# Kernel tuning notes

Hardware: AMD Instinct MI355X
Metric: run time of the kernel (lower is better)

The kernel has to match this reference:

```python
import jax, jax.numpy as jnp
import numpy as np

N_ATOMS = 50000
N_EDGES = 1_600_000
N_MOL = 500
HIDDEN = 128
FILTERS = 128
GAUSS = 50
LAYERS = 3
CUTOFF = 10.0
LOG2 = 0.6931471805599453


def ssp(x):
    # ShiftedSoftplus: softplus(x) - log(2)
    return jax.nn.softplus(x) - LOG2


def setup_inputs() -> dict:
    key = jax.random.key(0)
    ks = jax.random.split(key, 24)
    z = jax.random.randint(ks[0], (N_ATOMS,), 0, 100)
    pos = jax.random.uniform(ks[1], (N_ATOMS, 3), jnp.float32) * 5.0  # box keeps d < cutoff
    batch = jnp.sort(jax.random.randint(ks[2], (N_ATOMS,), 0, N_MOL))
    row = jax.random.randint(ks[3], (N_EDGES,), 0, N_ATOMS)
    off = jax.random.randint(ks[4], (N_EDGES,), 1, N_ATOMS)
    col = (row + off) % N_ATOMS  # guarantees row != col (no zero distances)
    edge_index = jnp.stack([row, col])
    def lin(k, fi, fo):
        return jax.random.normal(k, (fi, fo), jnp.float32) * (1.0 / np.sqrt(fi))
    emb = jax.random.normal(ks[5], (100, HIDDEN), jnp.float32)
    mlp1_w = jnp.stack([lin(jax.random.fold_in(ks[6], i), GAUSS, FILTERS) for i in range(LAYERS)])
    mlp1_b = jnp.zeros((LAYERS, FILTERS), jnp.float32)
    mlp2_w = jnp.stack([lin(jax.random.fold_in(ks[7], i), FILTERS, FILTERS) for i in range(LAYERS)])
    mlp2_b = jnp.zeros((LAYERS, FILTERS), jnp.float32)
    lin1_w = jnp.stack([lin(jax.random.fold_in(ks[8], i), HIDDEN, FILTERS) for i in range(LAYERS)])
    lin2_w = jnp.stack([lin(jax.random.fold_in(ks[9], i), FILTERS, HIDDEN) for i in range(LAYERS)])
    lin2_b = jnp.zeros((LAYERS, HIDDEN), jnp.float32)
    int_w = jnp.stack([lin(jax.random.fold_in(ks[10], i), HIDDEN, HIDDEN) for i in range(LAYERS)])
    int_b = jnp.zeros((LAYERS, HIDDEN), jnp.float32)
    out1_w = lin(ks[11], HIDDEN, HIDDEN // 2)
    out1_b = jnp.zeros((HIDDEN // 2,), jnp.float32)
    out2_w = lin(ks[12], HIDDEN // 2, 1)
    out2_b = jnp.zeros((1,), jnp.float32)
    return {"z": z, "pos": pos, "batch": batch, "edge_index": edge_index,
            "emb": emb, "mlp1_w": mlp1_w, "mlp1_b": mlp1_b, "mlp2_w": mlp2_w, "mlp2_b": mlp2_b,
            "lin1_w": lin1_w, "lin2_w": lin2_w, "lin2_b": lin2_b, "int_w": int_w, "int_b": int_b,
            "out1_w": out1_w, "out1_b": out1_b, "out2_w": out2_w, "out2_b": out2_b}


def reference(z, pos, batch, edge_index, emb, mlp1_w, mlp1_b, mlp2_w, mlp2_b,
              lin1_w, lin2_w, lin2_b, int_w, int_b, out1_w, out1_b, out2_w, out2_b):
    row, col = edge_index[0], edge_index[1]  # source j, target i
    d = jnp.linalg.norm(pos[row] - pos[col], axis=-1)  # [E]
    # GaussianSmearing
    offset = jnp.linspace(0.0, CUTOFF, GAUSS)
    coeff = -0.5 / (offset[1] - offset[0]) ** 2
    rbf = jnp.exp(coeff * (d[:, None] - offset[None, :]) ** 2)  # [E, GAUSS]
    # cosine cutoff
    C = 0.5 * (jnp.cos(d * jnp.pi / CUTOFF) + 1.0)  # [E]
    h = emb[z]  # [N, H]
    for l in range(LAYERS):
        W = ssp(rbf @ mlp1_w[l] + mlp1_b[l]) @ mlp2_w[l] + mlp2_b[l]  # [E, F]
        W = W * C[:, None]
        x = h @ lin1_w[l]                 # [N, F]
        msg = x[row] * W                  # gather from source, per-edge filter
        agg = jax.ops.segment_sum(msg, col, num_segments=N_ATOMS)  # scatter-add to targets
        x = agg @ lin2_w[l] + lin2_b[l]
        x = ssp(x)
        x = x @ int_w[l] + int_b[l]
        h = h + x                         # residual
    h = ssp(h @ out1_w + out1_b)
    h = h @ out2_w + out2_b               # [N, 1] per-atom energy
    out = jax.ops.segment_sum(h[:, 0], batch, num_segments=N_MOL)  # 'add' readout
    return out.reshape(-1)
```

## Files before the change

kernel.cpp:

```cpp
#include <hip/hip_runtime.h>
#include <math.h>

#define HID 128
#define NGAUSS 50
#define TBL 2048
#define TBL2 8192
#define DMAX 8.6605f
#define LDX 136

typedef _Float16 h4 __attribute__((ext_vector_type(4)));
typedef _Float16 f16x8 __attribute__((ext_vector_type(8)));
typedef float f32x4 __attribute__((ext_vector_type(4)));

__device__ __forceinline__ float sspf(float x) {
  float ax = fabsf(x);
  return fmaxf(x, 0.0f) + log1pf(expf(-ax)) - 0.69314718055994530942f;
}

__global__ __launch_bounds__(128) void build_table_k(
    const float* __restrict__ w1, const float* __restrict__ b1,
    const float* __restrict__ w2, const float* __restrict__ b2,
    float* __restrict__ tab) {
  int l = blockIdx.x >> 11;
  int ti = blockIdx.x & (TBL - 1);
  int j = threadIdx.x;
  __shared__ float rbf[NGAUSS];
  __shared__ float v1[HID];
  const float step = DMAX / (float)(TBL - 1);
  float d = ti * step;
  if (j < NGAUSS) {
    const float gstep = 10.0f / 49.0f;
    const float gcoeff = -12.005f;
    float diff = d - j * gstep;
    rbf[j] = expf(gcoeff * diff * diff);
  }
  __syncthreads();
  float s = b1[l * HID + j];
  const float* w1p = w1 + l * NGAUSS * HID + j;
  for (int g = 0; g < NGAUSS; g++) s = fmaf(rbf[g], w1p[g * HID], s);
  v1[j] = sspf(s);
  __syncthreads();
  float s2 = b2[l * HID + j];
  const float* w2p = w2 + l * HID * HID + j;
  for (int k = 0; k < HID; k++) s2 = fmaf(v1[k], w2p[k * HID], s2);
  float C = 0.5f * (cosf(d * 0.3141592653589793f) + 1.0f);
  tab[((size_t)l * TBL + ti) * HID + j] = s2 * C;
}

__global__ __launch_bounds__(256) void upsample_k(
    const float* __restrict__ tab, _Float16* __restrict__ tabh) {
  int idx = blockIdx.x * 256 + threadIdx.x;
  if (idx >= 3 * TBL2 * HID) return;
  int ch = idx & 127;
  int i = (idx >> 7) & (TBL2 - 1);
  int l = idx >> 20;
  float t = (float)i * ((float)(TBL - 1) / (float)(TBL2 - 1));
  int i0 = min((int)t, TBL - 2);
  float f = t - (float)i0;
  const float* base = tab + ((size_t)l * TBL + i0) * HID + ch;
  tabh[idx] = (_Float16)fmaf(f, base[HID] - base[0], base[0]);
}

__global__ __launch_bounds__(256) void wtrans10_k(
    const float* __restrict__ lin1, const float* __restrict__ lin2,
    const float* __restrict__ intw, const float* __restrict__ out1w,
    _Float16* __restrict__ out) {
  int b = blockIdx.x;
  __shared__ _Float16 tile[128 * 130];
  int t = threadIdx.x;
  if (b < 9) {
    const float* src = (b < 3 ? lin1 : (b < 6 ? lin2 : intw)) + (size_t)(b % 3) * HID * HID;
    _Float16* dst = out + (size_t)b * HID * HID;
    for (int i = t; i < HID * HID; i += 256) tile[(i >> 7) * 130 + (i & 127)] = (_Float16)src[i];
    __syncthreads();
    for (int i = t; i < HID * HID; i += 256) dst[i] = tile[(i & 127) * 130 + (i >> 7)];
  } else {
    _Float16* dst = out + (size_t)9 * HID * HID;
    for (int i = t; i < 128 * 64; i += 256) tile[(i >> 6) * 66 + (i & 63)] = (_Float16)out1w[i];
    __syncthreads();
    for (int i = t; i < 64 * 128; i += 256) dst[i] = tile[(i & 127) * 66 + (i >> 7)];
  }
}

__global__ __launch_bounds__(256) void bcount_k(
    const int* __restrict__ col, int* __restrict__ bcount, int E, int nbuck) {
  __shared__ int hist[1024];
  int t = threadIdx.x;
  int e0 = blockIdx.x * 2048;
  for (int j = t; j < nbuck; j += 256) hist[j] = 0;
  __syncthreads();
#pragma unroll
  for (int u = 0; u < 8; u++) {
    int e = e0 + u * 256 + t;
    if (e < E) atomicAdd(&hist[col[e] >> 6], 1);
  }
  __syncthreads();
  for (int j = t; j < nbuck; j += 256)
    if (hist[j]) atomicAdd(&bcount[j], hist[j]);
}

__global__ __launch_bounds__(256) void bucket_scan_k(
    const int* __restrict__ bcount, int* __restrict__ bstart,
    int* __restrict__ bcur, int nbuck, int* __restrict__ starts, int N) {
  __shared__ int sh[256];
  int t = threadIdx.x;
  int chunk = (nbuck + 255) / 256;
  int b0 = t * chunk;
  int c[8];
  int s = 0;
  for (int j = 0; j < chunk; j++) {
    int idx = b0 + j;
    int v = (idx < nbuck) ? bcount[idx] : 0;
    c[j] = v;
    s += v;
  }
  sh[t] = s;
  __syncthreads();
  for (int o = 1; o < 256; o <<= 1) {
    int v = (t >= o) ? sh[t - o] : 0;
    __syncthreads();
    sh[t] += v;
    __syncthreads();
  }
  int p = (t == 0) ? 0 : sh[t - 1];
  for (int j = 0; j < chunk; j++) {
    int idx = b0 + j;
    if (idx < nbuck) {
      bstart[idx] = p;
      bcur[idx] = p;
      p += c[j];
    }
  }
  if (t == 255) {
    bstart[nbuck] = p;
    starts[N] = p;
  }
}

__global__ __launch_bounds__(256) void scatterA_k(
    const int* __restrict__ row, const int* __restrict__ col,
    const float* __restrict__ pos, int* __restrict__ bcur,
    unsigned long long* __restrict__ tmp, int E, int nbuck) {
  __shared__ int hist[1024];
  __shared__ int base[1024];
  int t = threadIdx.x;
  int e0 = blockIdx.x * 2048;
  for (int j = t; j < nbuck; j += 256) hist[j] = 0;
  __syncthreads();
  int bkt[8];
  int rnk[8];
  unsigned long long key[8];
#pragma unroll
  for (int u = 0; u < 8; u++) {
    int e = e0 + u * 256 + t;
    bkt[u] = -1;
    if (e < E) {
      int r = row[e], c = col[e];
      float dx = pos[r * 3 + 0] - pos[c * 3 + 0];
      float dy = pos[r * 3 + 1] - pos[c * 3 + 1];
      float dz = pos[r * 3 + 2] - pos[c * 3 + 2];
      float d = sqrtf(dx * dx + dy * dy + dz * dz);
      const float inv2 = (float)(TBL2 - 1) / DMAX;
      int q = min((int)(d * inv2 + 0.5f), TBL2 - 1);
      unsigned int pay = ((unsigned int)r << 13) | (unsigned int)q;
      key[u] = ((unsigned long long)pay << 6) | (unsigned long long)(c & 63);
      bkt[u] = c >> 6;
      rnk[u] = atomicAdd(&hist[bkt[u]], 1);
    }
  }
  __syncthreads();
  for (int j = t; j < nbuck; j += 256)
    base[j] = hist[j] ? atomicAdd(&bcur[j], hist[j]) : 0;
  __syncthreads();
#pragma unroll
  for (int u = 0; u < 8; u++)
    if (bkt[u] >= 0) tmp[(size_t)base[bkt[u]] + rnk[u]] = key[u];
}

__global__ __launch_bounds__(256) void scatterB_k(
    const unsigned long long* __restrict__ tmp, const int* __restrict__ bstart,
    int* __restrict__ starts, unsigned int* __restrict__ payload, int N) {
  int j = blockIdx.x;
  int t = threadIdx.x;
  __shared__ int cnt[64];
  __shared__ int cur[64];
  int rs = bstart[j], re = bstart[j + 1];
  if (t < 64) cnt[t] = 0;
  __syncthreads();
  for (int e = rs + t; e < re; e += 256)
    atomicAdd(&cnt[(int)(tmp[e] & 63)], 1);
  __syncthreads();
  if (t < 64) {
    int mine = cnt[t];
    int v = mine;
    for (int o = 1; o < 64; o <<= 1) {
      int u = __shfl_up(v, o, 64);
      if (t >= o) v += u;
    }
    int excl = v - mine;
    int c = j * 64 + t;
    if (c < N) starts[c] = rs + excl;
    cur[t] = rs + excl;
  }
  __syncthreads();
  for (int e = rs + t; e < re; e += 256) {
    unsigned long long k = tmp[e];
    int p = atomicAdd(&cur[(int)(k & 63)], 1);
    payload[p] = (unsigned int)(k >> 6);
  }
}


__global__ __launch_bounds__(256) void lin1_emb_k(
    const int* __restrict__ z, const float* __restrict__ emb,
    const _Float16* __restrict__ W1t, float* __restrict__ h,
    _Float16* __restrict__ x16, int N) {
  __shared__ __align__(16) _Float16 Xs[32 * LDX];
  __shared__ __align__(16) _Float16 Ys[32 * LDX];
  __shared__ int zi[32];
  int t = threadIdx.x;
  int lane = t & 63, w = t >> 6;
  int g = w & 1, c = w >> 1;
  int mrow = lane & 15, quad = lane >> 4;
  int a0 = blockIdx.x * 32;
  if (t < 32) zi[t] = (a0 + t < N) ? z[a0 + t] : 0;
  __syncthreads();
#pragma unroll
  for (int p = 0; p < 4; p++) {
    int id = t + p * 256;
    int a = id >> 5, kg = id & 31;
    float4 v = ((const float4*)emb)[(size_t)zi[a] * 32 + kg];
    if (a0 + a < N) ((float4*)h)[(size_t)(a0 + a) * 32 + kg] = v;
    h4 o;
    o.x = (_Float16)v.x; o.y = (_Float16)v.y;
    o.z = (_Float16)v.z; o.w = (_Float16)v.w;
    *(h4*)&Xs[a * LDX + kg * 4] = o;
  }
  __syncthreads();
  f16x8 af[4];
#pragma unroll
  for (int kk = 0; kk < 4; kk++)
    af[kk] = *(const f16x8*)&Xs[(g * 16 + mrow) * LDX + kk * 32 + quad * 8];
  f32x4 zero = {0.f, 0.f, 0.f, 0.f};
  f32x4 acc[4];
#pragma unroll
  for (int i = 0; i < 4; i++) acc[i] = zero;
#pragma unroll
  for (int kk = 0; kk < 4; kk++) {
    f16x8 bf[4];
#pragma unroll
    for (int nt = 0; nt < 4; nt++)
      bf[nt] = *(const f16x8*)(W1t + (size_t)(c * 64 + nt * 16 + mrow) * HID + kk * 32 + quad * 8);
#pragma unroll
    for (int nt = 0; nt < 4; nt++)
      acc[nt] = __builtin_amdgcn_mfma_f32_16x16x32_f16(af[kk], bf[nt], acc[nt], 0, 0, 0);
  }
#pragma unroll
  for (int nt = 0; nt < 4; nt++) {
    int colv = c * 64 + nt * 16 + mrow;
#pragma unroll
    for (int r = 0; r < 4; r++)
      Ys[(g * 16 + quad * 4 + r) * LDX + colv] = (_Float16)acc[nt][r];
  }
  __syncthreads();
#pragma unroll
  for (int p = 0; p < 2; p++) {
    int id = t + p * 256;
    int a = id >> 4, kg = id & 15;
    if (a0 + a < N)
      ((uint4*)x16)[(size_t)(a0 + a) * 16 + kg] = *(uint4*)&Ys[a * LDX + kg * 8];
  }
}

__global__ __launch_bounds__(256) void fused_mid_k(
    const _Float16* __restrict__ agg16, const _Float16* __restrict__ W2t,
    const float* __restrict__ b2, const _Float16* __restrict__ W3t,
    const float* __restrict__ b3, float* __restrict__ h,
    const _Float16* __restrict__ W1nt, _Float16* __restrict__ x16, int N) {
  __shared__ __align__(16) _Float16 Xs[32 * LDX];
  __shared__ __align__(16) _Float16 Ys[32 * LDX];
  int t = threadIdx.x;
  int lane = t & 63, w = t >> 6;
  int g = w & 1, c = w >> 1;
  int mrow = lane & 15, quad = lane >> 4;
  int a0 = blockIdx.x * 32;
#pragma unroll
  for (int p = 0; p < 2; p++) {
    int id = t + p * 256;
    int a = id >> 4, kg = id & 15;
    uint4 v = make_uint4(0, 0, 0, 0);
    if (a0 + a < N) v = ((const uint4*)agg16)[(size_t)(a0 + a) * 16 + kg];
    *(uint4*)&Xs[a * LDX + kg * 8] = v;
  }
  __syncthreads();
  f32x4 zero = {0.f, 0.f, 0.f, 0.f};
  f16x8 af[4];
  f32x4 acc[4];
#pragma unroll
  for (int kk = 0; kk < 4; kk++)
    af[kk] = *(const f16x8*)&Xs[(g * 16 + mrow) * LDX + kk * 32 + quad * 8];
#pragma unroll
  for (int i = 0; i < 4; i++) acc[i] = zero;
#pragma unroll
  for (int kk = 0; kk < 4; kk++) {
    f16x8 bf[4];
#pragma unroll
    for (int nt = 0; nt < 4; nt++)
      bf[nt] = *(const f16x8*)(W2t + (size_t)(c * 64 + nt * 16 + mrow) * HID + kk * 32 + quad * 8);
#pragma unroll
    for (int nt = 0; nt < 4; nt++)
      acc[nt] = __builtin_amdgcn_mfma_f32_16x16x32_f16(af[kk], bf[nt], acc[nt], 0, 0, 0);
  }
#pragma unroll
  for (int nt = 0; nt < 4; nt++) {
    int colv = c * 64 + nt * 16 + mrow;
    float bb = b2[colv];
#pragma unroll
    for (int r = 0; r < 4; r++)
      Ys[(g * 16 + quad * 4 + r) * LDX + colv] = (_Float16)sspf(acc[nt][r] + bb);
  }
  __syncthreads();
#pragma unroll
  for (int kk = 0; kk < 4; kk++)
    af[kk] = *(const f16x8*)&Ys[(g * 16 + mrow) * LDX + kk * 32 + quad * 8];
#pragma unroll
  for (int i = 0; i < 4; i++) acc[i] = zero;
#pragma unroll
  for (int kk = 0; kk < 4; kk++) {
    f16x8 bf[4];
#pragma unroll
    for (int nt = 0; nt < 4; nt++)
      bf[nt] = *(const f16x8*)(W3t + (size_t)(c * 64 + nt * 16 + mrow) * HID + kk * 32 + quad * 8);
#pragma unroll
    for (int nt = 0; nt < 4; nt++)
      acc[nt] = __builtin_amdgcn_mfma_f32_16x16x32_f16(af[kk], bf[nt], acc[nt], 0, 0, 0);
  }
#pragma unroll
  for (int nt = 0; nt < 4; nt++) {
    int colv = c * 64 + nt * 16 + mrow;
    float bb = b3[colv];
#pragma unroll
    for (int r = 0; r < 4; r++)
      Xs[(g * 16 + quad * 4 + r) * LDX + colv] = (_Float16)(acc[nt][r] + bb);
  }
  __syncthreads();
#pragma unroll
  for (int p = 0; p < 4; p++) {
    int id = t + p * 256;
    int a = id >> 5, kg = id & 31;
    h4 xv = *(h4*)&Xs[a * LDX + kg * 4];
    float4 v = make_float4((float)xv.x, (float)xv.y, (float)xv.z, (float)xv.w);
    if (a0 + a < N) {
      float4 ho = ((const float4*)h)[(size_t)(a0 + a) * 32 + kg];
      v.x += ho.x; v.y += ho.y; v.z += ho.z; v.w += ho.w;
      ((float4*)h)[(size_t)(a0 + a) * 32 + kg] = v;
    }
    h4 o;
    o.x = (_Float16)v.x; o.y = (_Float16)v.y;
    o.z = (_Float16)v.z; o.w = (_Float16)v.w;
    *(h4*)&Xs[a * LDX + kg * 4] = o;
  }
  __syncthreads();
#pragma unroll
  for (int kk = 0; kk < 4; kk++)
    af[kk] = *(const f16x8*)&Xs[(g * 16 + mrow) * LDX + kk * 32 + quad * 8];
#pragma unroll
  for (int i = 0; i < 4; i++) acc[i] = zero;
#pragma unroll
  for (int kk = 0; kk < 4; kk++) {
    f16x8 bf[4];
#pragma unroll
    for (int nt = 0; nt < 4; nt++)
      bf[nt] = *(const f16x8*)(W1nt + (size_t)(c * 64 + nt * 16 + mrow) * HID + kk * 32 + quad * 8);
#pragma unroll
    for (int nt = 0; nt < 4; nt++)
      acc[nt] = __builtin_amdgcn_mfma_f32_16x16x32_f16(af[kk], bf[nt], acc[nt], 0, 0, 0);
  }
#pragma unroll
  for (int nt = 0; nt < 4; nt++) {
    int colv = c * 64 + nt * 16 + mrow;
#pragma unroll
    for (int r = 0; r < 4; r++)
      Ys[(g * 16 + quad * 4 + r) * LDX + colv] = (_Float16)acc[nt][r];
  }
  __syncthreads();
#pragma unroll
  for (int p = 0; p < 2; p++) {
    int id = t + p * 256;
    int a = id >> 4, kg = id & 15;
    if (a0 + a < N)
      ((uint4*)x16)[(size_t)(a0 + a) * 16 + kg] = *(uint4*)&Ys[a * LDX + kg * 8];
  }
}

__global__ __launch_bounds__(256) void fused_last_k(
    const _Float16* __restrict__ agg16, const _Float16* __restrict__ W2t,
    const float* __restrict__ b2, const _Float16* __restrict__ W3t,
    const float* __restrict__ b3, const float* __restrict__ h,
    const _Float16* __restrict__ Wo1t, const float* __restrict__ o1b,
    const float* __restrict__ o2w, const float* __restrict__ o2b,
    const int* __restrict__ batch, float* __restrict__ out, int N) {
  __shared__ __align__(16) _Float16 Xs[32 * LDX];
  __shared__ __align__(16) _Float16 Ys[32 * LDX];
  __shared__ float ebuf[32];
  int t = threadIdx.x;
  int lane = t & 63, w = t >> 6;
  int g = w & 1, c = w >> 1;
  int mrow = lane & 15, quad = lane >> 4;
  int a0 = blockIdx.x * 32;
  if (t < 32) ebuf[t] = 0.f;
#pragma unroll
  for (int p = 0; p < 2; p++) {
    int id = t + p * 256;
    int a = id >> 4, kg = id & 15;
    uint4 v = make_uint4(0, 0, 0, 0);
    if (a0 + a < N) v = ((const uint4*)agg16)[(size_t)(a0 + a) * 16 + kg];
    *(uint4*)&Xs[a * LDX + kg * 8] = v;
  }
  __syncthreads();
  f32x4 zero = {0.f, 0.f, 0.f, 0.f};
  f16x8 af[4];
  f32x4 acc[4];
#pragma unroll
  for (int kk = 0; kk < 4; kk++)
    af[kk] = *(const f16x8*)&Xs[(g * 16 + mrow) * LDX + kk * 32 + quad * 8];
#pragma unroll
  for (int i = 0; i < 4; i++) acc[i] = zero;
#pragma unroll
  for (int kk = 0; kk < 4; kk++) {
    f16x8 bf[4];
#pragma unroll
    for (int nt = 0; nt < 4; nt++)
      bf[nt] = *(const f16x8*)(W2t + (size_t)(c * 64 + nt * 16 + mrow) * HID + kk * 32 + quad * 8);
#pragma unroll
    for (int nt = 0; nt < 4; nt++)
      acc[nt] = __builtin_amdgcn_mfma_f32_16x16x32_f16(af[kk], bf[nt], acc[nt], 0, 0, 0);
  }
#pragma unroll
  for (int nt = 0; nt < 4; nt++) {
    int colv = c * 64 + nt * 16 + mrow;
    float bb = b2[colv];
#pragma unroll
    for (int r = 0; r < 4; r++)
      Ys[(g * 16 + quad * 4 + r) * LDX + colv] = (_Float16)sspf(acc[nt][r] + bb);
  }
  __syncthreads();
#pragma unroll
  for (int kk = 0; kk < 4; kk++)
    af[kk] = *(const f16x8*)&Ys[(g * 16 + mrow) * LDX + kk * 32 + quad * 8];
#pragma unroll
  for (int i = 0; i < 4; i++) acc[i] = zero;
#pragma unroll
  for (int kk = 0; kk < 4; kk++) {
    f16x8 bf[4];
#pragma unroll
    for (int nt = 0; nt < 4; nt++)
      bf[nt] = *(const f16x8*)(W3t + (size_t)(c * 64 + nt * 16 + mrow) * HID + kk * 32 + quad * 8);
#pragma unroll
    for (int nt = 0; nt < 4; nt++)
      acc[nt] = __builtin_amdgcn_mfma_f32_16x16x32_f16(af[kk], bf[nt], acc[nt], 0, 0, 0);
  }
#pragma unroll
  for (int nt = 0; nt < 4; nt++) {
    int colv = c * 64 + nt * 16 + mrow;
    float bb = b3[colv];
#pragma unroll
    for (int r = 0; r < 4; r++)
      Xs[(g * 16 + quad * 4 + r) * LDX + colv] = (_Float16)(acc[nt][r] + bb);
  }
  __syncthreads();
#pragma unroll
  for (int p = 0; p < 4; p++) {
    int id = t + p * 256;
    int a = id >> 5, kg = id & 31;
    h4 xv = *(h4*)&Xs[a * LDX + kg * 4];
    float4 v = make_float4((float)xv.x, (float)xv.y, (float)xv.z, (float)xv.w);
    if (a0 + a < N) {
      float4 ho = ((const float4*)h)[(size_t)(a0 + a) * 32 + kg];
      v.x += ho.x; v.y += ho.y; v.z += ho.z; v.w += ho.w;
    }
    h4 o;
    o.x = (_Float16)v.x; o.y = (_Float16)v.y;
    o.z = (_Float16)v.z; o.w = (_Float16)v.w;
    *(h4*)&Xs[a * LDX + kg * 4] = o;
  }
  __syncthreads();
#pragma unroll
  for (int kk = 0; kk < 4; kk++)
    af[kk] = *(const f16x8*)&Xs[(g * 16 + mrow) * LDX + kk * 32 + quad * 8];
#pragma unroll
  for (int i = 0; i < 2; i++) acc[i] = zero;
#pragma unroll
  for (int kk = 0; kk < 4; kk++) {
    f16x8 bf[2];
#pragma unroll
    for (int nt = 0; nt < 2; nt++)
      bf[nt] = *(const f16x8*)(Wo1t + (size_t)(c * 32 + nt * 16 + mrow) * HID + kk * 32 + quad * 8);
#pragma unroll
    for (int nt = 0; nt < 2; nt++)
      acc[nt] = __builtin_amdgcn_mfma_f32_16x16x32_f16(af[kk], bf[nt], acc[nt], 0, 0, 0);
  }
  float ss[4] = {0.f, 0.f, 0.f, 0.f};
#pragma unroll
  for (int nt = 0; nt < 2; nt++) {
    int colv = c * 32 + nt * 16 + mrow;
    float bb = o1b[colv];
    float ww = o2w[colv];
#pragma unroll
    for (int r = 0; r < 4; r++) ss[r] += sspf(acc[nt][r] + bb) * ww;
  }
#pragma unroll
  for (int r = 0; r < 4; r++) {
    ss[r] += __shfl_xor(ss[r], 1);
    ss[r] += __shfl_xor(ss[r], 2);
    ss[r] += __shfl_xor(ss[r], 4);
    ss[r] += __shfl_xor(ss[r], 8);
    if (mrow == 0) atomicAdd(&ebuf[g * 16 + quad * 4 + r], ss[r]);
  }
  __syncthreads();
  if (t < 32) {
    int a = a0 + t;
    if (a < N) atomicAdd(&out[batch[a]], ebuf[t] + o2b[0]);
  }
}

__global__ __launch_bounds__(256) void aggregate_k(
    const int* __restrict__ starts, const unsigned int* __restrict__ payload,
    const _Float16* __restrict__ x16, const _Float16* __restrict__ tabh,
    _Float16* __restrict__ agg16, int N) {
  int a = blockIdx.x * 4 + (threadIdx.x >> 6);
  if (a >= N) return;
  int lane = threadIdx.x & 63;
  int half = lane >> 5;
  int sl = lane & 31;
  int s = starts[a], e_end = starts[a + 1];
  float4 acc0 = make_float4(0.f, 0.f, 0.f, 0.f);
  float4 acc1 = make_float4(0.f, 0.f, 0.f, 0.f);
  auto do_edge = [&](unsigned int p, float4& acc) {
    int tq = (int)(p & 8191u);
    int r = (int)(p >> 13);
    h4 tw = *(const h4*)&tabh[(size_t)tq * HID + sl * 4];
    h4 xr = *(const h4*)&x16[(size_t)r * HID + sl * 4];
    acc.x = fmaf((float)xr.x, (float)tw.x, acc.x);
    acc.y = fmaf((float)xr.y, (float)tw.y, acc.y);
    acc.z = fmaf((float)xr.z, (float)tw.z, acc.z);
    acc.w = fmaf((float)xr.w, (float)tw.w, acc.w);
  };
  int i = s;
  for (; i + 8 <= e_end; i += 8) {
    unsigned int p0 = payload[i + half];
    unsigned int p1 = payload[i + 2 + half];
    unsigned int p2 = payload[i + 4 + half];
    unsigned int p3 = payload[i + 6 + half];
    do_edge(p0, acc0);
    do_edge(p1, acc1);
    do_edge(p2, acc0);
    do_edge(p3, acc1);
  }
  for (; i < e_end; i += 2) {
    int e = i + half;
    if (e < e_end) do_edge(payload[e], acc0);
  }
  acc0.x += acc1.x; acc0.y += acc1.y; acc0.z += acc1.z; acc0.w += acc1.w;
  acc0.x += __shfl_xor(acc0.x, 32);
  acc0.y += __shfl_xor(acc0.y, 32);
  acc0.z += __shfl_xor(acc0.z, 32);
  acc0.w += __shfl_xor(acc0.w, 32);
  if (half == 0) {
    h4 o;
    o.x = (_Float16)acc0.x; o.y = (_Float16)acc0.y;
    o.z = (_Float16)acc0.z; o.w = (_Float16)acc0.w;
    *(h4*)&agg16[(size_t)a * HID + sl * 4] = o;
  }
}

extern "C" void kernel_launch(void* const* d_in, const int* in_sizes, int n_in,
                              void* d_out, int out_size, void* d_ws, size_t ws_size,
                              hipStream_t stream) {
  const int* z = (const int*)d_in[0];
  const float* pos = (const float*)d_in[1];
  const int* batch = (const int*)d_in[2];
  const int* eidx = (const int*)d_in[3];
  const float* emb = (const float*)d_in[4];
  const float* mlp1_w = (const float*)d_in[5];
  const float* mlp1_b = (const float*)d_in[6];
  const float* mlp2_w = (const float*)d_in[7];
  const float* mlp2_b = (const float*)d_in[8];
  const float* lin1_w = (const float*)d_in[9];
  const float* lin2_w = (const float*)d_in[10];
  const float* lin2_b = (const float*)d_in[11];
  const float* int_w = (const float*)d_in[12];
  const float* int_b = (const float*)d_in[13];
  const float* out1_w = (const float*)d_in[14];
  const float* out1_b = (const float*)d_in[15];
  const float* out2_w = (const float*)d_in[16];
  const float* out2_b = (const float*)d_in[17];
  float* out = (float*)d_out;

  const int N = in_sizes[0];
  const int E = in_sizes[3] / 2;
  const int* row = eidx;
  const int* col = eidx + E;
  const int nbuck = (N + 63) / 64;

  char* ws = (char*)d_ws;
  size_t off = 0;
  auto alloc = [&](size_t bytes) -> void* {
    void* p = ws + off;
    off = (off + bytes + 255) & ~(size_t)255;
    return p;
  };
  float* h = (float*)alloc((size_t)N * HID * 4);
  _Float16* x16 = (_Float16*)alloc((size_t)N * HID * 2);
  size_t agg_bytes = (size_t)N * HID * 2;
  size_t tmp_bytes = (size_t)E * 8 + 16;
  void* agg_union = alloc(agg_bytes > tmp_bytes ? agg_bytes : tmp_bytes);
  _Float16* agg16 = (_Float16*)agg_union;
  unsigned long long* tmp = (unsigned long long*)agg_union;
  unsigned int* payload = (unsigned int*)alloc((size_t)E * 4 + 16);
  int* starts = (int*)alloc((size_t)(N + 1) * 4);
  int* bcount = (int*)alloc((size_t)nbuck * 4);
  int* bstart = (int*)alloc((size_t)(nbuck + 1) * 4);
  int* bcur = (int*)alloc((size_t)nbuck * 4);
  float* tab = (float*)alloc((size_t)3 * TBL * HID * 4);
  _Float16* tabh = (_Float16*)alloc((size_t)3 * TBL2 * HID * 2);
  _Float16* Wt10 = (_Float16*)alloc((size_t)10 * HID * HID * 2);
  (void)ws_size;

  hipMemsetAsync(bcount, 0, (size_t)nbuck * 4, stream);
  hipMemsetAsync(out, 0, (size_t)out_size * 4, stream);

  build_table_k<<<3 * TBL, 128, 0, stream>>>(mlp1_w, mlp1_b, mlp2_w, mlp2_b, tab);
  upsample_k<<<(3 * TBL2 * HID + 255) / 256, 256, 0, stream>>>(tab, tabh);
  wtrans10_k<<<10, 256, 0, stream>>>(lin1_w, lin2_w, int_w, out1_w, Wt10);
  bcount_k<<<(E + 2047) / 2048, 256, 0, stream>>>(col, bcount, E, nbuck);
  bucket_scan_k<<<1, 256, 0, stream>>>(bcount, bstart, bcur, nbuck, starts, N);
  scatterA_k<<<(E + 2047) / 2048, 256, 0, stream>>>(row, col, pos, bcur, tmp, E, nbuck);
  scatterB_k<<<nbuck, 256, 0, stream>>>(tmp, bstart, starts, payload, N);

  int g32 = (N + 31) / 32;
  lin1_emb_k<<<g32, 256, 0, stream>>>(z, emb, Wt10, h, x16, N);
  for (int l = 0; l < 2; l++) {
    aggregate_k<<<(N + 3) / 4, 256, 0, stream>>>(starts, payload, x16,
                                                 tabh + (size_t)l * TBL2 * HID, agg16, N);
    fused_mid_k<<<g32, 256, 0, stream>>>(
        agg16, Wt10 + (size_t)(3 + l) * HID * HID, lin2_b + (size_t)l * HID,
        Wt10 + (size_t)(6 + l) * HID * HID, int_b + (size_t)l * HID, h,
        Wt10 + (size_t)(l + 1) * HID * HID, x16, N);
  }
  aggregate_k<<<(N + 3) / 4, 256, 0, stream>>>(starts, payload, x16,
                                               tabh + (size_t)2 * TBL2 * HID, agg16, N);
  fused_last_k<<<g32, 256, 0, stream>>>(
      agg16, Wt10 + (size_t)5 * HID * HID, lin2_b + (size_t)2 * HID,
      Wt10 + (size_t)8 * HID * HID, int_b + (size_t)2 * HID, h,
      Wt10 + (size_t)9 * HID * HID, out1_b, out2_w, out2_b, batch, out, N);
}
```

Measured before the change: 617.5 us.

## Split fused node GEMMs into persistent kernels with LDS-resident swizzled weights

Weights are pre-swizzled into per-lane MFMA fragment order so each persistent block can load a whole 128x128 fp16 matrix into LDS once and reuse it across many 32-atom tiles. This replaces reading B fragments from global memory for every tile. The previously fused mid/last kernels are split into separate lin1, ssp, residual and energy kernels, and the embedding gather becomes its own kernel. The split adds launches and extra HBM round trips of intermediates (x16, h read/written more often) in exchange for weight reuse and fewer blocks.

```diff
diff --git a/kernel.cpp b/kernel.cpp
--- a/kernel.cpp
+++ b/kernel.cpp
@@ -7,6 +7,7 @@
 #define TBL2 8192
 #define DMAX 8.6605f
 #define LDX 136
+#define PGRID 768
 
 typedef _Float16 h4 __attribute__((ext_vector_type(4)));
 typedef _Float16 f16x8 __attribute__((ext_vector_type(8)));
@@ -61,25 +62,45 @@
   tabh[idx] = (_Float16)fmaf(f, base[HID] - base[0], base[0]);
 }
 
-__global__ __launch_bounds__(256) void wtrans10_k(
+__global__ __launch_bounds__(256) void wswz10_k(
     const float* __restrict__ lin1, const float* __restrict__ lin2,
     const float* __restrict__ intw, const float* __restrict__ out1w,
     _Float16* __restrict__ out) {
   int b = blockIdx.x;
-  __shared__ _Float16 tile[128 * 130];
   int t = threadIdx.x;
   if (b < 9) {
     const float* src = (b < 3 ? lin1 : (b < 6 ? lin2 : intw)) + (size_t)(b % 3) * HID * HID;
-    _Float16* dst = out + (size_t)b * HID * HID;
-    for (int i = t; i < HID * HID; i += 256) tile[(i >> 7) * 130 + (i & 127)] = (_Float16)src[i];
-    __syncthreads();
-    for (int i = t; i < HID * HID; i += 256) dst[i] = tile[(i & 127) * 130 + (i >> 7)];
+    _Float16* dst = out + (size_t)b * 16384;
+    for (int i = t; i < 16384; i += 256) {
+      int j = i & 7;
+      int lane = (i >> 3) & 63;
+      int kk = (i >> 9) & 3;
+      int ntc = i >> 11;
+      int n = ntc * 16 + (lane & 15);
+      int k = kk * 32 + (lane >> 4) * 8 + j;
+      dst[i] = (_Float16)src[k * HID + n];
+    }
   } else {
-    _Float16* dst = out + (size_t)9 * HID * HID;
-    for (int i = t; i < 128 * 64; i += 256) tile[(i >> 6) * 66 + (i & 63)] = (_Float16)out1w[i];
-    __syncthreads();
-    for (int i = t; i < 64 * 128; i += 256) dst[i] = tile[(i & 127) * 66 + (i >> 7)];
-  }
+    _Float16* dst = out + (size_t)9 * 16384;
+    for (int i = t; i < 8192; i += 256) {
+      int j = i & 7;
+      int lane = (i >> 3) & 63;
+      int kk = (i >> 9) & 3;
+      int ntc = i >> 11;
+      int n = ntc * 16 + (lane & 15);
+      int k = kk * 32 + (lane >> 4) * 8 + j;
+      dst[i] = (_Float16)out1w[k * 64 + n];
+    }
+  }
+}
+
+__global__ __launch_bounds__(256) void emb_gather_k(
+    const int* __restrict__ z, const float* __restrict__ emb,
+    float* __restrict__ h, int N) {
+  int i4 = blockIdx.x * 256 + threadIdx.x;
+  if (i4 >= N * 32) return;
+  int a = i4 >> 5;
+  ((float4*)h)[i4] = ((const float4*)emb)[z[a] * 32 + (i4 & 31)];
 }
 
 __global__ __launch_bounds__(256) void bcount_k(
@@ -211,316 +232,270 @@
 }
 
 
-__global__ __launch_bounds__(256) void lin1_emb_k(
-    const int* __restrict__ z, const float* __restrict__ emb,
-    const _Float16* __restrict__ W1t, float* __restrict__ h,
-    _Float16* __restrict__ x16, int N) {
+__global__ __launch_bounds__(256) void lin1_p_k(
+    const float* __restrict__ h, const _Float16* __restrict__ Wsw,
+    _Float16* __restrict__ x16, int N, int ntiles) {
+  __shared__ __align__(16) _Float16 Ws[16384];
   __shared__ __align__(16) _Float16 Xs[32 * LDX];
   __shared__ __align__(16) _Float16 Ys[32 * LDX];
-  __shared__ int zi[32];
   int t = threadIdx.x;
   int lane = t & 63, w = t >> 6;
   int g = w & 1, c = w >> 1;
   int mrow = lane & 15, quad = lane >> 4;
-  int a0 = blockIdx.x * 32;
-  if (t < 32) zi[t] = (a0 + t < N) ? z[a0 + t] : 0;
-  __syncthreads();
-#pragma unroll
-  for (int p = 0; p < 4; p++) {
-    int id = t + p * 256;
-    int a = id >> 5, kg = id & 31;
-    float4 v = ((const float4*)emb)[(size_t)zi[a] * 32 + kg];
-    if (a0 + a < N) ((float4*)h)[(size_t)(a0 + a) * 32 + kg] = v;
-    h4 o;
-    o.x = (_Float16)v.x; o.y = (_Float16)v.y;
-    o.z = (_Float16)v.z; o.w = (_Float16)v.w;
-    *(h4*)&Xs[a * LDX + kg * 4] = o;
-  }
-  __syncthreads();
-  f16x8 af[4];
-#pragma unroll
-  for (int kk = 0; kk < 4; kk++)
-    af[kk] = *(const f16x8*)&Xs[(g * 16 + mrow) * LDX + kk * 32 + quad * 8];
+#pragma unroll
+  for (int p = 0; p < 8; p++)
+    ((uint4*)Ws)[t + p * 256] = ((const uint4*)Wsw)[t + p * 256];
+  __syncthreads();
   f32x4 zero = {0.f, 0.f, 0.f, 0.f};
-  f32x4 acc[4];
-#pragma unroll
-  for (int i = 0; i < 4; i++) acc[i] = zero;
-#pragma unroll
-  for (int kk = 0; kk < 4; kk++) {
-    f16x8 bf[4];
-#pragma unroll
-    for (int nt = 0; nt < 4; nt++)
-      bf[nt] = *(const f16x8*)(W1t + (size_t)(c * 64 + nt * 16 + mrow) * HID + kk * 32 + quad * 8);
-#pragma unroll
-    for (int nt = 0; nt < 4; nt++)
-      acc[nt] = __builtin_amdgcn_mfma_f32_16x16x32_f16(af[kk], bf[nt], acc[nt], 0, 0, 0);
-  }
-#pragma unroll
-  for (int nt = 0; nt < 4; nt++) {
-    int colv = c * 64 + nt * 16 + mrow;
-#pragma unroll
-    for (int r = 0; r < 4; r++)
-      Ys[(g * 16 + quad * 4 + r) * LDX + colv] = (_Float16)acc[nt][r];
-  }
-  __syncthreads();
-#pragma unroll
-  for (int p = 0; p < 2; p++) {
-    int id = t + p * 256;
-    int a = id >> 4, kg = id & 15;
-    if (a0 + a < N)
-      ((uint4*)x16)[(size_t)(a0 + a) * 16 + kg] = *(uint4*)&Ys[a * LDX + kg * 8];
-  }
-}
-
-__global__ __launch_bounds__(256) void fused_mid_k(
-    const _Float16* __restrict__ agg16, const _Float16* __restrict__ W2t,
-    const float* __restrict__ b2, const _Float16* __restrict__ W3t,
-    const float* __restrict__ b3, float* __restrict__ h,
-    const _Float16* __restrict__ W1nt, _Float16* __restrict__ x16, int N) {
+  for (int tile = blockIdx.x; tile < ntiles; tile += gridDim.x) {
+    int a0 = tile * 32;
+#pragma unroll
+    for (int p = 0; p < 4; p++) {
+      int id = t + p * 256;
+      int a = id >> 5, kg = id & 31;
+      float4 v = make_float4(0.f, 0.f, 0.f, 0.f);
+      if (a0 + a < N) v = ((const float4*)h)[(size_t)(a0 + a) * 32 + kg];
+      h4 o;
+      o.x = (_Float16)v.x; o.y = (_Float16)v.y;
+      o.z = (_Float16)v.z; o.w = (_Float16)v.w;
+      *(h4*)&Xs[a * LDX + kg * 4] = o;
+    }
+    __syncthreads();
+    f16x8 af[4];
+#pragma unroll
+    for (int kk = 0; kk < 4; kk++)
+      af[kk] = *(const f16x8*)&Xs[(g * 16 + mrow) * LDX + kk * 32 + quad * 8];
+    f32x4 acc[4];
+#pragma unroll
+    for (int i = 0; i < 4; i++) acc[i] = zero;
+#pragma unroll
+    for (int kk = 0; kk < 4; kk++) {
+#pragma unroll
+      for (int nt = 0; nt < 4; nt++) {
+        f16x8 bf = *(const f16x8*)&Ws[(((c * 4 + nt) * 4 + kk) << 9) + lane * 8];
+        acc[nt] = __builtin_amdgcn_mfma_f32_16x16x32_f16(af[kk], bf, acc[nt], 0, 0, 0);
+      }
+    }
+#pragma unroll
+    for (int nt = 0; nt < 4; nt++) {
+      int colv = c * 64 + nt * 16 + mrow;
+#pragma unroll
+      for (int r = 0; r < 4; r++)
+        Ys[(g * 16 + quad * 4 + r) * LDX + colv] = (_Float16)acc[nt][r];
+    }
+    __syncthreads();
+#pragma unroll
+    for (int p = 0; p < 2; p++) {
+      int id = t + p * 256;
+      int a = id >> 4, kg = id & 15;
+      if (a0 + a < N)
+        ((uint4*)x16)[(size_t)(a0 + a) * 16 + kg] = *(uint4*)&Ys[a * LDX + kg * 8];
+    }
+  }
+}
+
+__global__ __launch_bounds__(256) void ssp_p_k(
+    const _Float16* __restrict__ agg16, const _Float16* __restrict__ Wsw,
+    const float* __restrict__ bias, _Float16* __restrict__ y16, int N, int ntiles) {
+  __shared__ __align__(16) _Float16 Ws[16384];
   __shared__ __align__(16) _Float16 Xs[32 * LDX];
   __shared__ __align__(16) _Float16 Ys[32 * LDX];
   int t = threadIdx.x;
   int lane = t & 63, w = t >> 6;
   int g = w & 1, c = w >> 1;
   int mrow = lane & 15, quad = lane >> 4;
-  int a0 = blockIdx.x * 32;
-#pragma unroll
-  for (int p = 0; p < 2; p++) {
-    int id = t + p * 256;
-    int a = id >> 4, kg = id & 15;
-    uint4 v = make_uint4(0, 0, 0, 0);
-    if (a0 + a < N) v = ((const uint4*)agg16)[(size_t)(a0 + a) * 16 + kg];
-    *(uint4*)&Xs[a * LDX + kg * 8] = v;
-  }
+#pragma unroll
+  for (int p = 0; p < 8; p++)
+    ((uint4*)Ws)[t + p * 256] = ((const uint4*)Wsw)[t + p * 256];
+  float br[4];
+#pragma unroll
+  for (int nt = 0; nt < 4; nt++) br[nt] = bias[c * 64 + nt * 16 + mrow];
   __syncthreads();
   f32x4 zero = {0.f, 0.f, 0.f, 0.f};
-  f16x8 af[4];
-  f32x4 acc[4];
-#pragma unroll
-  for (int kk = 0; kk < 4; kk++)
-    af[kk] = *(const f16x8*)&Xs[(g * 16 + mrow) * LDX + kk * 32 + quad * 8];
-#pragma unroll
-  for (int i = 0; i < 4; i++) acc[i] = zero;
-#pragma unroll
-  for (int kk = 0; kk < 4; kk++) {
-    f16x8 bf[4];
-#pragma unroll
-    for (int nt = 0; nt < 4; nt++)
-      bf[nt] = *(const f16x8*)(W2t + (size_t)(c * 64 + nt * 16 + mrow) * HID + kk * 32 + quad * 8);
-#pragma unroll
-    for (int nt = 0; nt < 4; nt++)
-      acc[nt] = __builtin_amdgcn_mfma_f32_16x16x32_f16(af[kk], bf[nt], acc[nt], 0, 0, 0);
-  }
-#pragma unroll
-  for (int nt = 0; nt < 4; nt++) {
-    int colv = c * 64 + nt * 16 + mrow;
-    float bb = b2[colv];
-#pragma unroll
-    for (int r = 0; r < 4; r++)
-      Ys[(g * 16 + quad * 4 + r) * LDX + colv] = (_Float16)sspf(acc[nt][r] + bb);
-  }
-  __syncthreads();
-#pragma unroll
-  for (int kk = 0; kk < 4; kk++)
-    af[kk] = *(const f16x8*)&Ys[(g * 16 + mrow) * LDX + kk * 32 + quad * 8];
-#pragma unroll
-  for (int i = 0; i < 4; i++) acc[i] = zero;
-#pragma unroll
-  for (int kk = 0; kk < 4; kk++) {
-    f16x8 bf[4];
-#pragma unroll
-    for (int nt = 0; nt < 4; nt++)
-      bf[nt] = *(const f16x8*)(W3t + (size_t)(c * 64 + nt * 16 + mrow) * HID + kk * 32 + quad * 8);
-#pragma unroll
-    for (int nt = 0; nt < 4; nt++)
-      acc[nt] = __builtin_amdgcn_mfma_f32_16x16x32_f16(af[kk], bf[nt], acc[nt], 0, 0, 0);
-  }
-#pragma unroll
-  for (int nt = 0; nt < 4; nt++) {
-    int colv = c * 64 + nt * 16 + mrow;
-    float bb = b3[colv];
-#pragma unroll
-    for (int r = 0; r < 4; r++)
-      Xs[(g * 16 + quad * 4 + r) * LDX + colv] = (_Float16)(acc[nt][r] + bb);
-  }
-  __syncthreads();
-#pragma unroll
-  for (int p = 0; p < 4; p++) {
-    int id = t + p * 256;
-    int a = id >> 5, kg = id & 31;
-    h4 xv = *(h4*)&Xs[a * LDX + kg * 4];
-    float4 v = make_float4((float)xv.x, (float)xv.y, (float)xv.z, (float)xv.w);
-    if (a0 + a < N) {
-      float4 ho = ((const float4*)h)[(size_t)(a0 + a) * 32 + kg];
-      v.x += ho.x; v.y += ho.y; v.z += ho.z; v.w += ho.w;
-      ((float4*)h)[(size_t)(a0 + a) * 32 + kg] = v;
-    }
-    h4 o;
-    o.x = (_Float16)v.x; o.y = (_Float16)v.y;
-    o.z = (_Float16)v.z; o.w = (_Float16)v.w;
-    *(h4*)&Xs[a * LDX + kg * 4] = o;
-  }
-  __syncthreads();
-#pragma unroll
-  for (int kk = 0; kk < 4; kk++)
-    af[kk] = *(const f16x8*)&Xs[(g * 16 + mrow) * LDX + kk * 32 + quad * 8];
-#pragma unroll
-  for (int i = 0; i < 4; i++) acc[i] = zero;
-#pragma unroll
-  for (int kk = 0; kk < 4; kk++) {
-    f16x8 bf[4];
-#pragma unroll
-    for (int nt = 0; nt < 4; nt++)
-      bf[nt] = *(const f16x8*)(W1nt + (size_t)(c * 64 + nt * 16 + mrow) * HID + kk * 32 + quad * 8);
-#pragma unroll
-    for (int nt = 0; nt < 4; nt++)
-      acc[nt] = __builtin_amdgcn_mfma_f32_16x16x32_f16(af[kk], bf[nt], acc[nt], 0, 0, 0);
-  }
-#pragma unroll
-  for (int nt = 0; nt < 4; nt++) {
-    int colv = c * 64 + nt * 16 + mrow;
-#pragma unroll
-    for (int r = 0; r < 4; r++)
-      Ys[(g * 16 + quad * 4 + r) * LDX + colv] = (_Float16)acc[nt][r];
-  }
-  __syncthreads();
-#pragma unroll
-  for (int p = 0; p < 2; p++) {
-    int id = t + p * 256;
-    int a = id >> 4, kg = id & 15;
-    if (a0 + a < N)
-      ((uint4*)x16)[(size_t)(a0 + a) * 16 + kg] = *(uint4*)&Ys[a * LDX + kg * 8];
-  }
-}
-
-__global__ __launch_bounds__(256) void fused_last_k(
-    const _Float16* __restrict__ agg16, const _Float16* __restrict__ W2t,
-    const float* __restrict__ b2, const _Float16* __restrict__ W3t,
-    const float* __restrict__ b3, const float* __restrict__ h,
-    const _Float16* __restrict__ Wo1t, const float* __restrict__ o1b,
-    const float* __restrict__ o2w, const float* __restrict__ o2b,
-    const int* __restrict__ batch, float* __restrict__ out, int N) {
+  for (int tile = blockIdx.x; tile < ntiles; tile += gridDim.x) {
+    int a0 = tile * 32;
+#pragma unroll
+    for (int p = 0; p < 2; p++) {
+      int id = t + p * 256;
+      int a = id >> 4, kg = id & 15;
+      uint4 v = make_uint4(0, 0, 0, 0);
+      if (a0 + a < N) v = ((const uint4*)agg16)[(size_t)(a0 + a) * 16 + kg];
+      *(uint4*)&Xs[a * LDX + kg * 8] = v;
+    }
+    __syncthreads();
+    f16x8 af[4];
+#pragma unroll
+    for (int kk = 0; kk < 4; kk++)
+      af[kk] = *(const f16x8*)&Xs[(g * 16 + mrow) * LDX + kk * 32 + quad * 8];
+    f32x4 acc[4];
+#pragma unroll
+    for (int i = 0; i < 4; i++) acc[i] = zero;
+#pragma unroll
+    for (int kk = 0; kk < 4; kk++) {
+#pragma unroll
+      for (int nt = 0; nt < 4; nt++) {
+        f16x8 bf = *(const f16x8*)&Ws[(((c * 4 + nt) * 4 + kk) << 9) + lane * 8];
+        acc[nt] = __builtin_amdgcn_mfma_f32_16x16x32_f16(af[kk], bf, acc[nt], 0, 0, 0);
+      }
+    }
+#pragma unroll
+    for (int nt = 0; nt < 4; nt++) {
+      int colv = c * 64 + nt * 16 + mrow;
+#pragma unroll
+      for (int r = 0; r < 4; r++)
+        Ys[(g * 16 + quad * 4 + r) * LDX + colv] = (_Float16)sspf(acc[nt][r] + br[nt]);
+    }
+    __syncthreads();
+#pragma unroll
+    for (int p = 0; p < 2; p++) {
+      int id = t + p * 256;
+      int a = id >> 4, kg = id & 15;
+      if (a0 + a < N)
+        ((uint4*)y16)[(size_t)(a0 + a) * 16 + kg] = *(uint4*)&Ys[a * LDX + kg * 8];
+    }
+  }
+}
+
+__global__ __launch_bounds__(256) void res_p_k(
+    const _Float16* __restrict__ y16, const _Float16* __restrict__ Wsw,
+    const float* __restrict__ bias, float* __restrict__ h, int N, int ntiles) {
+  __shared__ __align__(16) _Float16 Ws[16384];
   __shared__ __align__(16) _Float16 Xs[32 * LDX];
   __shared__ __align__(16) _Float16 Ys[32 * LDX];
-  __shared__ float ebuf[32];
   int t = threadIdx.x;
   int lane = t & 63, w = t >> 6;
   int g = w & 1, c = w >> 1;
   int mrow = lane & 15, quad = lane >> 4;
-  int a0 = blockIdx.x * 32;
-  if (t < 32) ebuf[t] = 0.f;
-#pragma unroll
-  for (int p = 0; p < 2; p++) {
-    int id = t + p * 256;
-    int a = id >> 4, kg = id & 15;
-    uint4 v = make_uint4(0, 0, 0, 0);
-    if (a0 + a < N) v = ((const uint4*)agg16)[(size_t)(a0 + a) * 16 + kg];
-    *(uint4*)&Xs[a * LDX + kg * 8] = v;
-  }
+#pragma unroll
+  for (int p = 0; p < 8; p++)
+    ((uint4*)Ws)[t + p * 256] = ((const uint4*)Wsw)[t + p * 256];
+  float br[4];
+#pragma unroll
+  for (int nt = 0; nt < 4; nt++) br[nt] = bias[c * 64 + nt * 16 + mrow];
   __syncthreads();
   f32x4 zero = {0.f, 0.f, 0.f, 0.f};
-  f16x8 af[4];
-  f32x4 acc[4];
-#pragma unroll
-  for (int kk = 0; kk < 4; kk++)
-    af[kk] = *(const f16x8*)&Xs[(g * 16 + mrow) * LDX + kk * 32 + quad * 8];
-#pragma unroll
-  for (int i = 0; i < 4; i++) acc[i] = zero;
-#pragma unroll
-  for (int kk = 0; kk < 4; kk++) {
-    f16x8 bf[4];
-#pragma unroll
-    for (int nt = 0; nt < 4; nt++)
-      bf[nt] = *(const f16x8*)(W2t + (size_t)(c * 64 + nt * 16 + mrow) * HID + kk * 32 + quad * 8);
-#pragma unroll
-    for (int nt = 0; nt < 4; nt++)
-      acc[nt] = __builtin_amdgcn_mfma_f32_16x16x32_f16(af[kk], bf[nt], acc[nt], 0, 0, 0);
-  }
-#pragma unroll
-  for (int nt = 0; nt < 4; nt++) {
-    int colv = c * 64 + nt * 16 + mrow;
-    float bb = b2[colv];
-#pragma unroll
-    for (int r = 0; r < 4; r++)
-      Ys[(g * 16 + quad * 4 + r) * LDX + colv] = (_Float16)sspf(acc[nt][r] + bb);
-  }
-  __syncthreads();
-#pragma unroll
-  for (int kk = 0; kk < 4; kk++)
-    af[kk] = *(const f16x8*)&Ys[(g * 16 + mrow) * LDX + kk * 32 + quad * 8];
-#pragma unroll
-  for (int i = 0; i < 4; i++) acc[i] = zero;
-#pragma unroll
-  for (int kk = 0; kk < 4; kk++) {
-    f16x8 bf[4];
-#pragma unroll
-    for (int nt = 0; nt < 4; nt++)
-      bf[nt] = *(const f16x8*)(W3t + (size_t)(c * 64 + nt * 16 + mrow) * HID + kk * 32 + quad * 8);
-#pragma unroll
-    for (int nt = 0; nt < 4; nt++)
-      acc[nt] = __builtin_amdgcn_mfma_f32_16x16x32_f16(af[kk], bf[nt], acc[nt], 0, 0, 0);
-  }
-#pragma unroll
-  for (int nt = 0; nt < 4; nt++) {
-    int colv = c * 64 + nt * 16 + mrow;
-    float bb = b3[colv];
-#pragma unroll
-    for (int r = 0; r < 4; r++)
-      Xs[(g * 16 + quad * 4 + r) * LDX + colv] = (_Float16)(acc[nt][r] + bb);
-  }
-  __syncthreads();
-#pragma unroll
-  for (int p = 0; p < 4; p++) {
-    int id = t + p * 256;
-    int a = id >> 5, kg = id & 31;
-    h4 xv = *(h4*)&Xs[a * LDX + kg * 4];
-    float4 v = make_float4((float)xv.x, (float)xv.y, (float)xv.z, (float)xv.w);
-    if (a0 + a < N) {
-      float4 ho = ((const float4*)h)[(size_t)(a0 + a) * 32 + kg];
-      v.x += ho.x; v.y += ho.y; v.z += ho.z; v.w += ho.w;
-    }
-    h4 o;
-    o.x = (_Float16)v.x; o.y = (_Float16)v.y;
-    o.z = (_Float16)v.z; o.w = (_Float16)v.w;
-    *(h4*)&Xs[a * LDX + kg * 4] = o;
-  }
-  __syncthreads();
-#pragma unroll
-  for (int kk = 0; kk < 4; kk++)
-    af[kk] = *(const f16x8*)&Xs[(g * 16 + mrow) * LDX + kk * 32 + quad * 8];
-#pragma unroll
-  for (int i = 0; i < 2; i++) acc[i] = zero;
-#pragma unroll
-  for (int kk = 0; kk < 4; kk++) {
-    f16x8 bf[2];
-#pragma unroll
-    for (int nt = 0; nt < 2; nt++)
-      bf[nt] = *(const f16x8*)(Wo1t + (size_t)(c * 32 + nt * 16 + mrow) * HID + kk * 32 + quad * 8);
-#pragma unroll
-    for (int nt = 0; nt < 2; nt++)
-      acc[nt] = __builtin_amdgcn_mfma_f32_16x16x32_f16(af[kk], bf[nt], acc[nt], 0, 0, 0);
-  }
-  float ss[4] = {0.f, 0.f, 0.f, 0.f};
+  for (int tile = blockIdx.x; tile < ntiles; tile += gridDim.x) {
+    int a0 = tile * 32;
+#pragma unroll
+    for (int p = 0; p < 2; p++) {
+      int id = t + p * 256;
+      int a = id >> 4, kg = id & 15;
+      uint4 v = make_uint4(0, 0, 0, 0);
+      if (a0 + a < N) v = ((const uint4*)y16)[(size_t)(a0 + a) * 16 + kg];
+      *(uint4*)&Xs[a * LDX + kg * 8] = v;
+    }
+    __syncthreads();
+    f16x8 af[4];
+#pragma unroll
+    for (int kk = 0; kk < 4; kk++)
+      af[kk] = *(const f16x8*)&Xs[(g * 16 + mrow) * LDX + kk * 32 + quad * 8];
+    f32x4 acc[4];
+#pragma unroll
+    for (int i = 0; i < 4; i++) acc[i] = zero;
+#pragma unroll
+    for (int kk = 0; kk < 4; kk++) {
+#pragma unroll
+      for (int nt = 0; nt < 4; nt++) {
+        f16x8 bf = *(const f16x8*)&Ws[(((c * 4 + nt) * 4 + kk) << 9) + lane * 8];
+        acc[nt] = __builtin_amdgcn_mfma_f32_16x16x32_f16(af[kk], bf, acc[nt], 0, 0, 0);
+      }
+    }
+#pragma unroll
+    for (int nt = 0; nt < 4; nt++) {
+      int colv = c * 64 + nt * 16 + mrow;
+#pragma unroll
+      for (int r = 0; r < 4; r++)
+        Ys[(g * 16 + quad * 4 + r) * LDX + colv] = (_Float16)(acc[nt][r] + br[nt]);
+    }
+    __syncthreads();
+#pragma unroll
+    for (int p = 0; p < 4; p++) {
+      int id = t + p * 256;
+      int a = id >> 5, kg = id & 31;
+      if (a0 + a < N) {
+        h4 yv = *(h4*)&Ys[a * LDX + kg * 4];
+        float4 ho = ((const float4*)h)[(size_t)(a0 + a) * 32 + kg];
+        ho.x += (float)yv.x; ho.y += (float)yv.y;
+        ho.z += (float)yv.z; ho.w += (float)yv.w;
+        ((float4*)h)[(size_t)(a0 + a) * 32 + kg] = ho;
+      }
+    }
+  }
+}
+
+__global__ __launch_bounds__(256) void energy_p_k(
+    const float* __restrict__ h, const _Float16* __restrict__ Wsw,
+    const float* __restrict__ o1b, const float* __restrict__ o2w,
+    const float* __restrict__ o2b, const int* __restrict__ batch,
+    float* __restrict__ out, int N, int ntiles) {
+  __shared__ __align__(16) _Float16 Ws[8192];
+  __shared__ __align__(16) _Float16 Xs[32 * LDX];
+  __shared__ float ebuf[32];
+  int t = threadIdx.x;
+  int lane = t & 63, w = t >> 6;
+  int g = w & 1, c = w >> 1;
+  int mrow = lane & 15, quad = lane >> 4;
+#pragma unroll
+  for (int p = 0; p < 4; p++)
+    ((uint4*)Ws)[t + p * 256] = ((const uint4*)Wsw)[t + p * 256];
+  float br[2], wr[2];
 #pragma unroll
   for (int nt = 0; nt < 2; nt++) {
     int colv = c * 32 + nt * 16 + mrow;
-    float bb = o1b[colv];
-    float ww = o2w[colv];
-#pragma unroll
-    for (int r = 0; r < 4; r++) ss[r] += sspf(acc[nt][r] + bb) * ww;
-  }
-#pragma unroll
-  for (int r = 0; r < 4; r++) {
-    ss[r] += __shfl_xor(ss[r], 1);
-    ss[r] += __shfl_xor(ss[r], 2);
-    ss[r] += __shfl_xor(ss[r], 4);
-    ss[r] += __shfl_xor(ss[r], 8);
-    if (mrow == 0) atomicAdd(&ebuf[g * 16 + quad * 4 + r], ss[r]);
-  }
-  __syncthreads();
-  if (t < 32) {
-    int a = a0 + t;
-    if (a < N) atomicAdd(&out[batch[a]], ebuf[t] + o2b[0]);
+    br[nt] = o1b[colv];
+    wr[nt] = o2w[colv];
+  }
+  float o2b0 = o2b[0];
+  if (t < 32) ebuf[t] = 0.f;
+  __syncthreads();
+  f32x4 zero = {0.f, 0.f, 0.f, 0.f};
+  for (int tile = blockIdx.x; tile < ntiles; tile += gridDim.x) {
+    int a0 = tile * 32;
+#pragma unroll
+    for (int p = 0; p < 4; p++) {
+      int id = t + p * 256;
+      int a = id >> 5, kg = id & 31;
+      float4 v = make_float4(0.f, 0.f, 0.f, 0.f);
+      if (a0 + a < N) v = ((const float4*)h)[(size_t)(a0 + a) * 32 + kg];
+      h4 o;
+      o.x = (_Float16)v.x; o.y = (_Float16)v.y;
+      o.z = (_Float16)v.z; o.w = (_Float16)v.w;
+      *(h4*)&Xs[a * LDX + kg * 4] = o;
+    }
+    __syncthreads();
+    f16x8 af[4];
+#pragma unroll
+    for (int kk = 0; kk < 4; kk++)
+      af[kk] = *(const f16x8*)&Xs[(g * 16 + mrow) * LDX + kk * 32 + quad * 8];
+    f32x4 acc[2];
+    acc[0] = zero; acc[1] = zero;
+#pragma unroll
+    for (int kk = 0; kk < 4; kk++) {
+#pragma unroll
+      for (int nt = 0; nt < 2; nt++) {
+        f16x8 bf = *(const f16x8*)&Ws[(((c * 2 + nt) * 4 + kk) << 9) + lane * 8];
+        acc[nt] = __builtin_amdgcn_mfma_f32_16x16x32_f16(af[kk], bf, acc[nt], 0, 0, 0);
+      }
+    }
+    float ss[4] = {0.f, 0.f, 0.f, 0.f};
+#pragma unroll
+    for (int nt = 0; nt < 2; nt++)
+#pragma unroll
+      for (int r = 0; r < 4; r++) ss[r] += sspf(acc[nt][r] + br[nt]) * wr[nt];
+#pragma unroll
+    for (int r = 0; r < 4; r++) {
+      ss[r] += __shfl_xor(ss[r], 1);
+      ss[r] += __shfl_xor(ss[r], 2);
+      ss[r] += __shfl_xor(ss[r], 4);
+      ss[r] += __shfl_xor(ss[r], 8);
+      if (mrow == 0) atomicAdd(&ebuf[g * 16 + quad * 4 + r], ss[r]);
+    }
+    __syncthreads();
+    if (t < 32) {
+      int a = a0 + t;
+      if (a < N) atomicAdd(&out[batch[a]], ebuf[t] + o2b0);
+      ebuf[t] = 0.f;
+    }
   }
 }
 
@@ -602,6 +577,7 @@
   const int* row = eidx;
   const int* col = eidx + E;
   const int nbuck = (N + 63) / 64;
+  const int ntiles = (N + 31) / 32;
 
   char* ws = (char*)d_ws;
   size_t off = 0;
@@ -624,7 +600,7 @@
   int* bcur = (int*)alloc((size_t)nbuck * 4);
   float* tab = (float*)alloc((size_t)3 * TBL * HID * 4);
   _Float16* tabh = (_Float16*)alloc((size_t)3 * TBL2 * HID * 2);
-  _Float16* Wt10 = (_Float16*)alloc((size_t)10 * HID * HID * 2);
+  _Float16* Wsw = (_Float16*)alloc((size_t)10 * 16384 * 2);
   (void)ws_size;
 
   hipMemsetAsync(bcount, 0, (size_t)nbuck * 4, stream);
@@ -632,26 +608,23 @@
 
   build_table_k<<<3 * TBL, 128, 0, stream>>>(mlp1_w, mlp1_b, mlp2_w, mlp2_b, tab);
   upsample_k<<<(3 * TBL2 * HID + 255) / 256, 256, 0, stream>>>(tab, tabh);
-  wtrans10_k<<<10, 256, 0, stream>>>(lin1_w, lin2_w, int_w, out1_w, Wt10);
+  wswz10_k<<<10, 256, 0, stream>>>(lin1_w, lin2_w, int_w, out1_w, Wsw);
+  emb_gather_k<<<(N * 32 + 255) / 256, 256, 0, stream>>>(z, emb, h, N);
   bcount_k<<<(E + 2047) / 2048, 256, 0, stream>>>(col, bcount, E, nbuck);
   bucket_scan_k<<<1, 256, 0, stream>>>(bcount, bstart, bcur, nbuck, starts, N);
   scatterA_k<<<(E + 2047) / 2048, 256, 0, stream>>>(row, col, pos, bcur, tmp, E, nbuck);
   scatterB_k<<<nbuck, 256, 0, stream>>>(tmp, bstart, starts, payload, N);
 
-  int g32 = (N + 31) / 32;
-  lin1_emb_k<<<g32, 256, 0, stream>>>(z, emb, Wt10, h, x16, N);
-  for (int l = 0; l < 2; l++) {
+  int pg = PGRID < ntiles ? PGRID : ntiles;
+  for (int l = 0; l < 3; l++) {
+    lin1_p_k<<<pg, 256, 0, stream>>>(h, Wsw + (size_t)l * 16384, x16, N, ntiles);
     aggregate_k<<<(N + 3) / 4, 256, 0, stream>>>(starts, payload, x16,
                                                  tabh + (size_t)l * TBL2 * HID, agg16, N);
-    fused_mid_k<<<g32, 256, 0, stream>>>(
-        agg16, Wt10 + (size_t)(3 + l) * HID * HID, lin2_b + (size_t)l * HID,
-        Wt10 + (size_t)(6 + l) * HID * HID, int_b + (size_t)l * HID, h,
-        Wt10 + (size_t)(l + 1) * HID * HID, x16, N);
-  }
-  aggregate_k<<<(N + 3) / 4, 256, 0, stream>>>(starts, payload, x16,
-                                               tabh + (size_t)2 * TBL2 * HID, agg16, N);
-  fused_last_k<<<g32, 256, 0, stream>>>(
-      agg16, Wt10 + (size_t)5 * HID * HID, lin2_b + (size_t)2 * HID,
-      Wt10 + (size_t)8 * HID * HID, int_b + (size_t)2 * HID, h,
-      Wt10 + (size_t)9 * HID * HID, out1_b, out2_w, out2_b, batch, out, N);
-}
+    ssp_p_k<<<pg, 256, 0, stream>>>(agg16, Wsw + (size_t)(3 + l) * 16384,
+                                    lin2_b + (size_t)l * HID, x16, N, ntiles);
+    res_p_k<<<pg, 256, 0, stream>>>(x16, Wsw + (size_t)(6 + l) * 16384,
+                                    int_b + (size_t)l * HID, h, N, ntiles);
+  }
+  energy_p_k<<<pg, 256, 0, stream>>>(h, Wsw + (size_t)9 * 16384, out1_b, out2_w,
+                                     out2_b, batch, out, N, ntiles);
+}
```

After: 620.7 us. Within noise of the previous version (+0.5%).
